# Optimization experiments

Measured on AMD Instinct MI355X. Metric: run time of the kernel, lower is better.

## Reference

```python
import jax, jax.numpy as jnp
import numpy as np

PI = np.pi


def setup_inputs() -> dict:
    key = jax.random.key(0)
    ks = jax.random.split(key, 20)
    B, L, D = 2, 1024, 512
    TP = 16      # n_sets(4) * planes_per_set(4)
    PP = 16      # pos_planes
    MAXL = 8192
    sc = 1.0 / np.sqrt(D)
    return {
        "x": jax.random.normal(ks[0], (B, L, D), jnp.float32),
        "Wk": jax.random.normal(ks[1], (TP, D), jnp.float32) * sc,
        "bk": jnp.zeros((TP,), jnp.float32),
        "Wq": jax.random.normal(ks[2], (TP, D), jnp.float32) * sc,
        "bq": jnp.zeros((TP,), jnp.float32),
        "Wv": jax.random.normal(ks[3], (D, D), jnp.float32) * sc,
        "bv": jnp.zeros((D,), jnp.float32),
        "ln_g": jnp.ones((D,), jnp.float32),
        "ln_b": jnp.zeros((D,), jnp.float32),
        "Wo": jax.random.normal(ks[4], (D, D), jnp.float32) * sc,
        "bo": jnp.zeros((D,), jnp.float32),
        "set_w": jnp.ones((4,), jnp.float32),
        "pos_phases": jax.random.normal(ks[5], (MAXL, PP), jnp.float32) * PI,
        "pos_weight": jnp.ones((1,), jnp.float32),
        "Wg1": jax.random.normal(ks[6], (D // 2, D), jnp.float32) * sc,
        "bg1": jnp.zeros((D // 2,), jnp.float32),
        "Wg2": jax.random.normal(ks[7], (1, D // 2), jnp.float32) * np.sqrt(2.0 / D),
        "bg2": jnp.zeros((1,), jnp.float32),
    }


def reference(x, Wk, bk, Wq, bq, Wv, bv, ln_g, ln_b, Wo, bo,
              set_w, pos_phases, pos_weight, Wg1, bg1, Wg2, bg2):
    B, L, D = x.shape
    n_sets, pps = 4, 4

    # --- content phasor memory ---
    kp = jnp.tanh(x @ Wk.T + bk) * PI                       # [B,L,16]
    qp = jnp.tanh(x @ Wq.T + bq) * PI
    key_ph = jnp.exp(1j * kp).reshape(B, L, n_sets, pps)    # [B,L,S,P] c64
    qry_ph = jnp.exp(1j * qp).reshape(B, L, n_sets, pps)
    Vr = x @ Wv.T + bv                                       # [B,L,D]
    V = Vr.astype(jnp.complex64)

    bound = key_ph[..., None] * V[:, :, None, None, :]       # [B,L,S,P,D] c64
    mem = jnp.cumsum(bound, axis=1)                          # prefix-sum memory
    retr = (mem * jnp.conj(qry_ph)[..., None]).sum(axis=3).real   # [B,L,S,D]
    w = jax.nn.softmax(set_w)
    content = (retr * w[None, None, :, None]).sum(axis=2)    # [B,L,D]

    # --- positional cos/sin memory ---
    ph = pos_phases[:L]                                      # [L,PP]
    c = jnp.cos(ph)[None]                                    # [1,L,PP]
    s = jnp.sin(ph)[None]
    br = Vr[:, :, None, :] * c[..., None]                    # [B,L,PP,D]
    bi = Vr[:, :, None, :] * s[..., None]
    mr = jnp.cumsum(br, axis=1)
    mi = jnp.cumsum(bi, axis=1)
    pos = (mr * c[..., None] + mi * s[..., None]).sum(axis=2)  # [B,L,D]

    # --- gate, mix, normalize, output proj ---
    g = jax.nn.sigmoid(
        jax.nn.gelu(x @ Wg1.T + bg1, approximate=False) @ Wg2.T + bg2)  # [B,L,1]
    total = g * content + (1.0 - g) * jax.nn.sigmoid(pos_weight) * pos
    norm = jnp.sqrt(jnp.arange(1, L + 1, dtype=x.dtype) * pps)[None, :, None]
    t = total / norm
    mu = t.mean(-1, keepdims=True)
    var = ((t - mu) ** 2).mean(-1, keepdims=True)
    tn = (t - mu) / jnp.sqrt(var + 1e-5) * ln_g + ln_b
    return x + tn @ Wo.T + bo
```

## Files before the change

kernel.cpp:

```cpp
#include <hip/hip_runtime.h>
#include <math.h>

#define PI_F 3.14159265358979323846f
#define BB 2
#define LL 1024
#define NCH 64
#define CHUNK 32
#define NCHUNK (LL/CHUNK)
#define NW 1408

typedef __attribute__((ext_vector_type(8))) short short8;
typedef __attribute__((ext_vector_type(4))) float floatx4;
typedef const __attribute__((address_space(1))) unsigned int cgu32;
typedef __attribute__((address_space(3))) unsigned int lu32;

__device__ __forceinline__ unsigned short f2bf(float f){
    unsigned u = __float_as_uint(f);
    unsigned r = (u + 0x7fff + ((u >> 16) & 1)) >> 16;
    return (unsigned short)r;
}

__global__ __launch_bounds__(128) void k_prep(
    const float* __restrict__ Wv, const float* __restrict__ Wg1,
    const float* __restrict__ Wk, const float* __restrict__ Wq,
    const float* __restrict__ Wo,
    const float* __restrict__ bv, const float* __restrict__ bg1,
    const float* __restrict__ bk, const float* __restrict__ bq,
    const float* __restrict__ bo, const float* __restrict__ x,
    unsigned short* __restrict__ Wb, float* __restrict__ bcat,
    unsigned short* __restrict__ xb)
{
    const int bid = blockIdx.x, tid = threadIdx.x;
    if (bid < NW){
        const int n = bid;
        const float* src = (n<512) ? Wv  + (size_t)n*512
                         : (n<768) ? Wg1 + (size_t)(n-512)*512
                         : (n<784) ? Wk  + (size_t)(n-768)*512
                         : (n<800) ? Wq  + (size_t)(n-784)*512
                         : (n<896) ? (const float*)0
                                   : Wo  + (size_t)(n-896)*512;
        float4 v = make_float4(0.f,0.f,0.f,0.f);
        if (src) v = ((const float4*)src)[tid];
        ushort4 o; o.x=f2bf(v.x); o.y=f2bf(v.y); o.z=f2bf(v.z); o.w=f2bf(v.w);
        ((ushort4*)(Wb + (size_t)n*512))[tid] = o;
        if (tid == 0)
            bcat[n] = (n<512)?bv[n] : (n<768)?bg1[n-512] : (n<784)?bk[n-768]
                    : (n<800)?bq[n-784] : (n<896)?0.f : bo[n-896];
    } else {
        const size_t i = (size_t)(bid - NW)*128 + tid;
        float4 v = ((const float4*)x)[i];
        ushort4 o; o.x=f2bf(v.x); o.y=f2bf(v.y); o.z=f2bf(v.z); o.w=f2bf(v.w);
        ((ushort4*)xb)[i] = o;
    }
}

__device__ __forceinline__ void gemm64x64(
    const unsigned short* Ag, const unsigned short* Bg,
    short* As, short* Bs, int tid, floatx4 acc[2][2])
{
    const int lane = tid & 63, w = tid >> 6;
    const int wm = w & 1, wn = w >> 1;
    const int q = lane >> 4, m15 = lane & 15;
    for (int kt = 0; kt < 512; kt += 64) {
        __syncthreads();
        #pragma unroll
        for (int i = 0; i < 2; ++i) {
            const int rowbase = (w*2 + i) * 8;
            const int r  = rowbase + (lane >> 3);
            const int gb = (lane & 7) ^ (r & 7);
            __builtin_amdgcn_global_load_lds(
                (cgu32*)(const void*)(Ag + (size_t)r*512 + kt + gb*8),
                (lu32*)(As + rowbase*64), 16, 0, 0);
            __builtin_amdgcn_global_load_lds(
                (cgu32*)(const void*)(Bg + (size_t)r*512 + kt + gb*8),
                (lu32*)(Bs + rowbase*64), 16, 0, 0);
        }
        __syncthreads();
        #pragma unroll
        for (int k32 = 0; k32 < 64; k32 += 32) {
            short8 af[2], bf[2];
            #pragma unroll
            for (int t = 0; t < 2; ++t) {
                const int ra  = 32*wm + 16*t + m15;
                const int sba = ((k32>>3) + q) ^ (ra & 7);
                af[t] = *(const short8*)(As + ra*64 + sba*8);
                const int rb  = 32*wn + 16*t + m15;
                const int sbb = ((k32>>3) + q) ^ (rb & 7);
                bf[t] = *(const short8*)(Bs + rb*64 + sbb*8);
            }
            #pragma unroll
            for (int mt = 0; mt < 2; ++mt)
                #pragma unroll
                for (int nt = 0; nt < 2; ++nt)
                    acc[mt][nt] = __builtin_amdgcn_mfma_f32_16x16x32_bf16(
                        af[mt], bf[nt], acc[mt][nt], 0, 0, 0);
        }
    }
}

__global__ __launch_bounds__(256,2) void kg1f(
    const unsigned short* __restrict__ xb, const unsigned short* __restrict__ Wb,
    const float* __restrict__ bcat, const float* __restrict__ Wg2,
    const float* __restrict__ bg2, const float* __restrict__ set_w,
    const float* __restrict__ pos_phases, const float* __restrict__ pos_weight,
    unsigned short* __restrict__ Vt,
    unsigned short* __restrict__ ab, unsigned short* __restrict__ Rb,
    unsigned short* __restrict__ aT)
{
    __shared__ short smem[22528];
    const int bid = blockIdx.x, tid = threadIdx.x;
    const int lane = tid & 63, w = tid >> 6;
    const int q = lane >> 4, m15 = lane & 15;

    if (bid < 256){
        short* As = smem;
        short* Bs = smem + 64*64;
        const int row0 = (bid >> 3)*64, n0 = (bid & 7)*64;
        floatx4 acc[2][2];
        #pragma unroll
        for (int mt=0;mt<2;++mt)
            #pragma unroll
            for (int nt=0;nt<2;++nt) acc[mt][nt] = (floatx4){0.f,0.f,0.f,0.f};
        gemm64x64(xb + (size_t)row0*512, Wb + (size_t)n0*512, As, Bs, tid, acc);
        const int wm = w & 1, wn = w >> 1;
        const int b = row0 >> 10, lb = row0 & 1023;
        #pragma unroll
        for (int mt=0;mt<2;++mt)
            #pragma unroll
            for (int nt=0;nt<2;++nt){
                const int d = n0 + 32*wn + 16*nt + m15;
                const float bb = bcat[d];
                const int l0 = lb + 32*wm + 16*mt + q*4;
                ushort4 o;
                o.x = f2bf(acc[mt][nt][0] + bb);
                o.y = f2bf(acc[mt][nt][1] + bb);
                o.z = f2bf(acc[mt][nt][2] + bb);
                o.w = f2bf(acc[mt][nt][3] + bb);
                *(ushort4*)(Vt + ((size_t)(b*512 + d))*1024 + l0) = o;
            }
    } else {
        short* As2 = smem;
        short* Bs2 = smem + 64*64;
        const int r0 = (bid - 256)*64;
        floatx4 acc2[18];
        #pragma unroll
        for (int nt=0;nt<18;++nt) acc2[nt] = (floatx4){0.f,0.f,0.f,0.f};
        for (int kt = 0; kt < 512; kt += 64){
            __syncthreads();
            #pragma unroll
            for (int i=0;i<2;++i){
                const int rowbase = (w*2 + i)*8;
                const int r = rowbase + (lane >> 3);
                const int gb = (lane & 7) ^ (r & 7);
                __builtin_amdgcn_global_load_lds(
                    (cgu32*)(const void*)(xb + (size_t)(r0 + r)*512 + kt + gb*8),
                    (lu32*)(As2 + rowbase*64), 16, 0, 0);
            }
            #pragma unroll
            for (int i=0;i<9;++i){
                const int rowbase = (w*9 + i)*8;
                const int r = rowbase + (lane >> 3);
                const int gb = (lane & 7) ^ (r & 7);
                __builtin_amdgcn_global_load_lds(
                    (cgu32*)(const void*)(Wb + (size_t)(512 + r)*512 + kt + gb*8),
                    (lu32*)(Bs2 + rowbase*64), 16, 0, 0);
            }
            __syncthreads();
            #pragma unroll
            for (int k32 = 0; k32 < 64; k32 += 32){
                const int ra  = 16*w + m15;
                const int sba = ((k32>>3) + q) ^ (ra & 7);
                short8 af = *(const short8*)(As2 + ra*64 + sba*8);
                #pragma unroll
                for (int nt=0;nt<18;++nt){
                    const int rb  = 16*nt + m15;
                    const int sbb = ((k32>>3) + q) ^ (rb & 7);
                    short8 bf = *(const short8*)(Bs2 + rb*64 + sbb*8);
                    acc2[nt] = __builtin_amdgcn_mfma_f32_16x16x32_bf16(
                        af, bf, acc2[nt], 0, 0, 0);
                }
            }
        }
        float s0=set_w[0], s1=set_w[1], s2=set_w[2], s3=set_w[3];
        float mx = fmaxf(fmaxf(s0,s1), fmaxf(s2,s3));
        float e0=expf(s0-mx), e1=expf(s1-mx), e2=expf(s2-mx), e3=expf(s3-mx);
        float esum = e0+e1+e2+e3;
        float spw = 1.f/(1.f+expf(-pos_weight[0]));
        float b2 = bg2[0];
        float part[4] = {0.f,0.f,0.f,0.f};
        #pragma unroll
        for (int nt=0;nt<16;++nt){
            const float w2 = Wg2[16*nt + m15];
            const float hb = bcat[512 + 16*nt + m15];
            #pragma unroll
            for (int reg=0;reg<4;++reg){
                float hv = acc2[nt][reg] + hb;
                float ge = 0.5f*hv*(1.f + erff(hv*0.70710678118f));
                part[reg] += ge*w2;
            }
        }
        #pragma unroll
        for (int off=8; off; off>>=1)
            #pragma unroll
            for (int reg=0;reg<4;++reg) part[reg] += __shfl_xor(part[reg], off, 64);
        const int j = m15;
        const float bkj = bcat[768 + j], bqj = bcat[784 + j];
        const float wsm = (j<4?e0: j<8?e1: j<12?e2: e3) / esum;
        #pragma unroll
        for (int reg=0;reg<4;++reg){
            const int row = r0 + 16*w + q*4 + reg;
            const int l = row & (LL-1), b = row >> 10;
            float g = 1.f/(1.f+expf(-(part[reg] + b2)));
            float kang = PI_F*tanhf(acc2[16][reg] + bkj);
            float qang = PI_F*tanhf(acc2[17][reg] + bqj);
            float rnorm = 1.f/(2.f*sqrtf((float)(l+1)));
            float av[4], rv[4];
            av[0] = cosf(kang); av[1] = sinf(kang);
            float cw = g*wsm*rnorm;
            rv[0] = cw*cosf(qang); rv[1] = cw*sinf(qang);
            float ph = pos_phases[(size_t)l*16 + j];
            float pc = cosf(ph), ps = sinf(ph);
            av[2] = pc; av[3] = ps;
            float cp = (1.f-g)*spw*rnorm;
            rv[2] = cp*pc; rv[3] = cp*ps;
            unsigned short* arow = ab + (size_t)row*NCH;
            unsigned short* Rrow = Rb + (size_t)row*NCH;
            #pragma unroll
            for (int t=0;t<4;++t){
                arow[16*t + j] = f2bf(av[t]);
                Rrow[16*t + j] = f2bf(rv[t]);
                aT[((size_t)(b*NCH + 16*t + j))*1024 + l] = f2bf(av[t]);
            }
        }
    }
}

__global__ __launch_bounds__(256) void k2a_chunksum(
    const unsigned short* __restrict__ aT, const unsigned short* __restrict__ Vt,
    float* __restrict__ P)
{
    const int c = blockIdx.x, b = blockIdx.y, z = blockIdx.z;
    const int tid = threadIdx.x, lane = tid & 63, w = tid >> 6;
    const int q = lane >> 4, m15 = lane & 15;
    short8 af[4];
    #pragma unroll
    for (int mt=0;mt<4;++mt)
        af[mt] = *(const short8*)(aT + ((size_t)b*NCH + 16*mt + m15)*1024 + c*32 + q*8);
    floatx4 acc[4][4];
    #pragma unroll
    for (int mt=0;mt<4;++mt)
        #pragma unroll
        for (int nt=0;nt<4;++nt) acc[mt][nt] = (floatx4){0.f,0.f,0.f,0.f};
    #pragma unroll
    for (int nt=0;nt<4;++nt){
        const int d = z*256 + w*64 + 16*nt + m15;
        short8 bf = *(const short8*)(Vt + ((size_t)(b*512 + d))*1024 + c*32 + q*8);
        #pragma unroll
        for (int mt=0;mt<4;++mt)
            acc[mt][nt] = __builtin_amdgcn_mfma_f32_16x16x32_bf16(af[mt], bf, acc[mt][nt], 0,0,0);
    }
    float* Pc = P + ((size_t)(b*NCHUNK + c))*512*NCH;
    #pragma unroll
    for (int mt=0;mt<4;++mt)
        #pragma unroll
        for (int nt=0;nt<4;++nt){
            const int d = z*256 + w*64 + 16*nt + m15;
            *(floatx4*)(Pc + (size_t)d*NCH + 16*mt + q*4) = acc[mt][nt];
        }
}

__global__ __launch_bounds__(256) void k2b_prefix(
    const float* __restrict__ P, unsigned short* __restrict__ S0t)
{
    const int b = blockIdx.y;
    const size_t idx = (size_t)blockIdx.x*256 + threadIdx.x;
    float run = 0.f;
    for (int c=0;c<NCHUNK;++c){
        const size_t o = ((size_t)(b*NCHUNK + c))*512*NCH + idx;
        float v = P[o];
        S0t[o] = f2bf(run);
        run += v;
    }
}

__global__ __launch_bounds__(256) void k2c_scan(
    const unsigned short* __restrict__ ab, const unsigned short* __restrict__ Rb,
    const unsigned short* __restrict__ Vt, const unsigned short* __restrict__ S0t,
    const float* __restrict__ ln_g, const float* __restrict__ ln_b,
    unsigned short* __restrict__ Tn)
{
    __shared__ short Msh[32*32];
    __shared__ float Tsh[32*512];
    const int c = blockIdx.x, b = blockIdx.y;
    const int tid = threadIdx.x, lane = tid & 63, w = tid >> 6;
    const int q = lane >> 4, m15 = lane & 15;
    const int grow = b*1024 + c*32;

    if (w == 0){
        floatx4 mcc[2][2];
        #pragma unroll
        for (int mt=0;mt<2;++mt)
            #pragma unroll
            for (int nt=0;nt<2;++nt) mcc[mt][nt] = (floatx4){0.f,0.f,0.f,0.f};
        #pragma unroll
        for (int ks=0;ks<2;++ks){
            short8 ra[2], bb[2];
            #pragma unroll
            for (int t=0;t<2;++t){
                ra[t] = *(const short8*)(Rb + (size_t)(grow + 16*t + m15)*NCH + ks*32 + q*8);
                bb[t] = *(const short8*)(ab + (size_t)(grow + 16*t + m15)*NCH + ks*32 + q*8);
            }
            #pragma unroll
            for (int mt=0;mt<2;++mt)
                #pragma unroll
                for (int nt=0;nt<2;++nt)
                    mcc[mt][nt] = __builtin_amdgcn_mfma_f32_16x16x32_bf16(
                        ra[mt], bb[nt], mcc[mt][nt], 0,0,0);
        }
        #pragma unroll
        for (int mt=0;mt<2;++mt)
            #pragma unroll
            for (int nt=0;nt<2;++nt){
                const int nl = 16*nt + m15;
                #pragma unroll
                for (int reg=0;reg<4;++reg){
                    const int ml = 16*mt + q*4 + reg;
                    Msh[ml*32 + nl] = (nl <= ml) ? (short)f2bf(mcc[mt][nt][reg]) : (short)0;
                }
            }
    }
    __syncthreads();

    short8 a1[2], a2[2][2];
    #pragma unroll
    for (int mt=0;mt<2;++mt){
        a1[mt] = *(const short8*)(Msh + (16*mt + m15)*32 + q*8);
        #pragma unroll
        for (int ks=0;ks<2;++ks)
            a2[ks][mt] = *(const short8*)(Rb + (size_t)(grow + 16*mt + m15)*NCH + ks*32 + q*8);
    }
    floatx4 acc[2][8];
    #pragma unroll
    for (int mt=0;mt<2;++mt)
        #pragma unroll
        for (int nt=0;nt<8;++nt) acc[mt][nt] = (floatx4){0.f,0.f,0.f,0.f};
    const unsigned short* S0c = S0t + ((size_t)(b*NCHUNK + c))*512*NCH;
    #pragma unroll
    for (int nt=0;nt<8;++nt){
        const int d = w*128 + 16*nt + m15;
        short8 b1 = *(const short8*)(Vt + ((size_t)(b*512 + d))*1024 + c*32 + q*8);
        #pragma unroll
        for (int mt=0;mt<2;++mt)
            acc[mt][nt] = __builtin_amdgcn_mfma_f32_16x16x32_bf16(a1[mt], b1, acc[mt][nt], 0,0,0);
        #pragma unroll
        for (int ks=0;ks<2;++ks){
            short8 b2 = *(const short8*)(S0c + (size_t)d*NCH + ks*32 + q*8);
            #pragma unroll
            for (int mt=0;mt<2;++mt)
                acc[mt][nt] = __builtin_amdgcn_mfma_f32_16x16x32_bf16(a2[ks][mt], b2, acc[mt][nt], 0,0,0);
        }
    }
    #pragma unroll
    for (int mt=0;mt<2;++mt)
        #pragma unroll
        for (int nt=0;nt<8;++nt){
            const int d = w*128 + 16*nt + m15;
            #pragma unroll
            for (int reg=0;reg<4;++reg)
                Tsh[(16*mt + q*4 + reg)*512 + d] = acc[mt][nt][reg];
        }
    __syncthreads();

    #pragma unroll
    for (int i=0;i<8;++i){
        const int r = w*8 + i;
        float s=0.f, sq=0.f;
        #pragma unroll
        for (int t=0;t<8;++t){
            float v = Tsh[r*512 + lane + 64*t];
            s += v; sq += v*v;
        }
        #pragma unroll
        for (int off=32; off; off>>=1){
            s += __shfl_xor(s, off, 64); sq += __shfl_xor(sq, off, 64);
        }
        float mu  = s*(1.f/512.f);
        float var = sq*(1.f/512.f) - mu*mu;
        float rsd = rsqrtf(var + 1e-5f);
        unsigned short* trow = Tn + (size_t)(grow + r)*512;
        #pragma unroll
        for (int t=0;t<8;++t){
            const int d = lane + 64*t;
            float v = (Tsh[r*512 + d] - mu)*rsd*ln_g[d] + ln_b[d];
            trow[d] = f2bf(v);
        }
    }
}

__global__ __launch_bounds__(256) void kg2(
    const unsigned short* __restrict__ Tn, const unsigned short* __restrict__ Wb,
    const float* __restrict__ bcat, const float* __restrict__ x,
    float* __restrict__ out)
{
    __shared__ short As[64*64], Bs[64*64];
    const int tid = threadIdx.x;
    const int row0 = blockIdx.x*64, n0 = blockIdx.y*64;
    floatx4 acc[2][2];
    #pragma unroll
    for (int mt=0;mt<2;++mt)
        #pragma unroll
        for (int nt=0;nt<2;++nt) acc[mt][nt] = (floatx4){0.f,0.f,0.f,0.f};
    gemm64x64(Tn + (size_t)row0*512, Wb + (size_t)(896+n0)*512, As, Bs, tid, acc);
    const int lane = tid & 63, w = tid >> 6;
    const int wm = w & 1, wn = w >> 1, q = lane >> 4, m15 = lane & 15;
    #pragma unroll
    for (int mt=0;mt<2;++mt)
        #pragma unroll
        for (int nt=0;nt<2;++nt){
            const int n = n0 + 32*wn + 16*nt + m15;
            const float bb = bcat[896 + n];
            #pragma unroll
            for (int reg=0;reg<4;++reg){
                const int m = row0 + 32*wm + 16*mt + q*4 + reg;
                out[(size_t)m*512 + n] = x[(size_t)m*512 + n] + acc[mt][nt][reg] + bb;
            }
        }
}

extern "C" void kernel_launch(void* const* d_in, const int* in_sizes, int n_in,
                              void* d_out, int out_size, void* d_ws, size_t ws_size,
                              hipStream_t stream) {
    const float* x    = (const float*)d_in[0];
    const float* Wk   = (const float*)d_in[1];
    const float* bk   = (const float*)d_in[2];
    const float* Wq   = (const float*)d_in[3];
    const float* bq   = (const float*)d_in[4];
    const float* Wv   = (const float*)d_in[5];
    const float* bv   = (const float*)d_in[6];
    const float* ln_g = (const float*)d_in[7];
    const float* ln_b = (const float*)d_in[8];
    const float* Wo   = (const float*)d_in[9];
    const float* bo   = (const float*)d_in[10];
    const float* set_w      = (const float*)d_in[11];
    const float* pos_phases = (const float*)d_in[12];
    const float* pos_weight = (const float*)d_in[13];
    const float* Wg1  = (const float*)d_in[14];
    const float* bg1  = (const float*)d_in[15];
    const float* Wg2  = (const float*)d_in[16];
    const float* bg2  = (const float*)d_in[17];
    float* out = (float*)d_out;

    float* ws   = (float*)d_ws;
    float* bcat = ws;
    float* P    = bcat + NW;
    unsigned short* Wb  = (unsigned short*)(P + (size_t)BB*NCHUNK*512*NCH);
    unsigned short* xb  = Wb  + (size_t)NW*512;
    unsigned short* Vt  = xb  + (size_t)2048*512;
    unsigned short* ab  = Vt  + (size_t)BB*512*1024;
    unsigned short* Rb  = ab  + (size_t)2048*NCH;
    unsigned short* aT  = Rb  + (size_t)2048*NCH;
    unsigned short* S0t = aT  + (size_t)BB*NCH*1024;
    unsigned short* Tn  = S0t + (size_t)BB*NCHUNK*512*NCH;

    k_prep<<<dim3(NW + 2048), 128, 0, stream>>>(
        Wv,Wg1,Wk,Wq,Wo, bv,bg1,bk,bq,bo, x, Wb, bcat, xb);
    kg1f<<<dim3(288), 256, 0, stream>>>(
        xb, Wb, bcat, Wg2, bg2, set_w, pos_phases, pos_weight, Vt, ab, Rb, aT);
    k2a_chunksum<<<dim3(NCHUNK, BB, 2), 256, 0, stream>>>(aT, Vt, P);
    k2b_prefix<<<dim3(512*NCH/256, BB), 256, 0, stream>>>(P, S0t);
    k2c_scan<<<dim3(NCHUNK, BB), 256, 0, stream>>>(ab, Rb, Vt, S0t, ln_g, ln_b, Tn);
    kg2<<<dim3(2048/64, 512/64), 256, 0, stream>>>(Tn, Wb, bcat, x, out);
}
```

Before: 148.5 us.

## Fold LayerNorm into output GEMM epilogue and widen scan grid

```diff
diff --git a/kernel.cpp b/kernel.cpp
--- a/kernel.cpp
+++ b/kernel.cpp
@@ -27,11 +27,14 @@
     const float* __restrict__ bv, const float* __restrict__ bg1,
     const float* __restrict__ bk, const float* __restrict__ bq,
     const float* __restrict__ bo, const float* __restrict__ x,
+    const float* __restrict__ ln_g, const float* __restrict__ ln_b,
     unsigned short* __restrict__ Wb, float* __restrict__ bcat,
+    float* __restrict__ Gv, float* __restrict__ Bv, float* __restrict__ stats,
     unsigned short* __restrict__ xb)
 {
     const int bid = blockIdx.x, tid = threadIdx.x;
     if (bid < NW){
+        if (bid < 32) stats[bid*128 + tid] = 0.f;
         const int n = bid;
         const float* src = (n<512) ? Wv  + (size_t)n*512
                          : (n<768) ? Wg1 + (size_t)(n-512)*512
@@ -41,11 +44,34 @@
                                    : Wo  + (size_t)(n-896)*512;
         float4 v = make_float4(0.f,0.f,0.f,0.f);
         if (src) v = ((const float4*)src)[tid];
-        ushort4 o; o.x=f2bf(v.x); o.y=f2bf(v.y); o.z=f2bf(v.z); o.w=f2bf(v.w);
-        ((ushort4*)(Wb + (size_t)n*512))[tid] = o;
+        if (n >= 896){
+            float4 g4 = ((const float4*)ln_g)[tid];
+            float4 b4 = ((const float4*)ln_b)[tid];
+            ushort4 o;
+            o.x=f2bf(v.x*g4.x); o.y=f2bf(v.y*g4.y);
+            o.z=f2bf(v.z*g4.z); o.w=f2bf(v.w*g4.w);
+            ((ushort4*)(Wb + (size_t)n*512))[tid] = o;
+            float pg = v.x*g4.x + v.y*g4.y + v.z*g4.z + v.w*g4.w;
+            float pb = v.x*b4.x + v.y*b4.y + v.z*b4.z + v.w*b4.w;
+            #pragma unroll
+            for (int off=32; off; off>>=1){
+                pg += __shfl_xor(pg, off, 64); pb += __shfl_xor(pb, off, 64);
+            }
+            __shared__ float red[4];
+            const int wv = tid >> 6;
+            if ((tid & 63) == 0){ red[wv*2] = pg; red[wv*2+1] = pb; }
+            __syncthreads();
+            if (tid == 0){
+                Gv[n-896] = red[0] + red[2];
+                Bv[n-896] = red[1] + red[3] + bo[n-896];
+            }
+        } else {
+            ushort4 o; o.x=f2bf(v.x); o.y=f2bf(v.y); o.z=f2bf(v.z); o.w=f2bf(v.w);
+            ((ushort4*)(Wb + (size_t)n*512))[tid] = o;
+        }
         if (tid == 0)
             bcat[n] = (n<512)?bv[n] : (n<768)?bg1[n-512] : (n<784)?bk[n-768]
-                    : (n<800)?bq[n-784] : (n<896)?0.f : bo[n-896];
+                    : (n<800)?bq[n-784] : 0.f;
     } else {
         const size_t i = (size_t)(bid - NW)*128 + tid;
         float4 v = ((const float4*)x)[i];
@@ -112,10 +138,11 @@
     const int lane = tid & 63, w = tid >> 6;
     const int q = lane >> 4, m15 = lane & 15;
 
-    if (bid < 256){
+    if (bid >= 32){
         short* As = smem;
         short* Bs = smem + 64*64;
-        const int row0 = (bid >> 3)*64, n0 = (bid & 7)*64;
+        const int vb = bid - 32;
+        const int row0 = (vb >> 3)*64, n0 = (vb & 7)*64;
         floatx4 acc[2][2];
         #pragma unroll
         for (int mt=0;mt<2;++mt)
@@ -141,7 +168,7 @@
     } else {
         short* As2 = smem;
         short* Bs2 = smem + 64*64;
-        const int r0 = (bid - 256)*64;
+        const int r0 = bid*64;
         floatx4 acc2[18];
         #pragma unroll
         for (int nt=0;nt<18;++nt) acc2[nt] = (floatx4){0.f,0.f,0.f,0.f};
@@ -246,14 +273,14 @@
     #pragma unroll
     for (int mt=0;mt<4;++mt)
         af[mt] = *(const short8*)(aT + ((size_t)b*NCH + 16*mt + m15)*1024 + c*32 + q*8);
-    floatx4 acc[4][4];
+    floatx4 acc[4][2];
     #pragma unroll
     for (int mt=0;mt<4;++mt)
         #pragma unroll
-        for (int nt=0;nt<4;++nt) acc[mt][nt] = (floatx4){0.f,0.f,0.f,0.f};
-    #pragma unroll
-    for (int nt=0;nt<4;++nt){
-        const int d = z*256 + w*64 + 16*nt + m15;
+        for (int nt=0;nt<2;++nt) acc[mt][nt] = (floatx4){0.f,0.f,0.f,0.f};
+    #pragma unroll
+    for (int nt=0;nt<2;++nt){
+        const int d = z*128 + w*32 + 16*nt + m15;
         short8 bf = *(const short8*)(Vt + ((size_t)(b*512 + d))*1024 + c*32 + q*8);
         #pragma unroll
         for (int mt=0;mt<4;++mt)
@@ -263,8 +290,8 @@
     #pragma unroll
     for (int mt=0;mt<4;++mt)
         #pragma unroll
-        for (int nt=0;nt<4;++nt){
-            const int d = z*256 + w*64 + 16*nt + m15;
+        for (int nt=0;nt<2;++nt){
+            const int d = z*128 + w*32 + 16*nt + m15;
             *(floatx4*)(Pc + (size_t)d*NCH + 16*mt + q*4) = acc[mt][nt];
         }
 }
@@ -274,132 +301,124 @@
 {
     const int b = blockIdx.y;
     const size_t idx = (size_t)blockIdx.x*256 + threadIdx.x;
+    const size_t base = (size_t)b*NCHUNK*512*NCH + idx;
+    float vcs[NCHUNK];
+    #pragma unroll
+    for (int c=0;c<NCHUNK;++c)
+        vcs[c] = P[base + (size_t)c*512*NCH];
     float run = 0.f;
+    #pragma unroll
     for (int c=0;c<NCHUNK;++c){
-        const size_t o = ((size_t)(b*NCHUNK + c))*512*NCH + idx;
-        float v = P[o];
-        S0t[o] = f2bf(run);
-        run += v;
+        S0t[base + (size_t)c*512*NCH] = f2bf(run);
+        run += vcs[c];
     }
 }
 
 __global__ __launch_bounds__(256) void k2c_scan(
     const unsigned short* __restrict__ ab, const unsigned short* __restrict__ Rb,
     const unsigned short* __restrict__ Vt, const unsigned short* __restrict__ S0t,
-    const float* __restrict__ ln_g, const float* __restrict__ ln_b,
-    unsigned short* __restrict__ Tn)
-{
-    __shared__ short Msh[32*32];
-    __shared__ float Tsh[32*512];
-    const int c = blockIdx.x, b = blockIdx.y;
+    unsigned short* __restrict__ Tn, float* __restrict__ stats)
+{
+    __shared__ short Msh[4][32*32];
+    const int c = blockIdx.x, b = blockIdx.y, z = blockIdx.z;
     const int tid = threadIdx.x, lane = tid & 63, w = tid >> 6;
     const int q = lane >> 4, m15 = lane & 15;
     const int grow = b*1024 + c*32;
 
-    if (w == 0){
-        floatx4 mcc[2][2];
+    short8 ra[2][2], av[2][2];
+    #pragma unroll
+    for (int ks=0;ks<2;++ks)
+        #pragma unroll
+        for (int t=0;t<2;++t){
+            ra[ks][t] = *(const short8*)(Rb + (size_t)(grow + 16*t + m15)*NCH + ks*32 + q*8);
+            av[ks][t] = *(const short8*)(ab + (size_t)(grow + 16*t + m15)*NCH + ks*32 + q*8);
+        }
+    floatx4 mcc[2][2];
+    #pragma unroll
+    for (int mt=0;mt<2;++mt)
+        #pragma unroll
+        for (int nt=0;nt<2;++nt) mcc[mt][nt] = (floatx4){0.f,0.f,0.f,0.f};
+    #pragma unroll
+    for (int ks=0;ks<2;++ks)
         #pragma unroll
         for (int mt=0;mt<2;++mt)
             #pragma unroll
-            for (int nt=0;nt<2;++nt) mcc[mt][nt] = (floatx4){0.f,0.f,0.f,0.f};
+            for (int nt=0;nt<2;++nt)
+                mcc[mt][nt] = __builtin_amdgcn_mfma_f32_16x16x32_bf16(
+                    ra[ks][mt], av[ks][nt], mcc[mt][nt], 0,0,0);
+    short* Mw = &Msh[w][0];
+    #pragma unroll
+    for (int mt=0;mt<2;++mt)
+        #pragma unroll
+        for (int nt=0;nt<2;++nt){
+            const int nl = 16*nt + m15;
+            #pragma unroll
+            for (int reg=0;reg<4;++reg){
+                const int ml = 16*mt + q*4 + reg;
+                Mw[ml*32 + nl] = (nl <= ml) ? (short)f2bf(mcc[mt][nt][reg]) : (short)0;
+            }
+        }
+    short8 a1[2];
+    #pragma unroll
+    for (int mt=0;mt<2;++mt)
+        a1[mt] = *(const short8*)(Mw + (16*mt + m15)*32 + q*8);
+
+    floatx4 acc[2][2];
+    #pragma unroll
+    for (int mt=0;mt<2;++mt)
+        #pragma unroll
+        for (int nt=0;nt<2;++nt) acc[mt][nt] = (floatx4){0.f,0.f,0.f,0.f};
+    const unsigned short* S0c = S0t + ((size_t)(b*NCHUNK + c))*512*NCH;
+    #pragma unroll
+    for (int nt=0;nt<2;++nt){
+        const int d = z*128 + w*32 + 16*nt + m15;
+        short8 vfr = *(const short8*)(Vt + ((size_t)(b*512 + d))*1024 + c*32 + q*8);
+        #pragma unroll
+        for (int mt=0;mt<2;++mt)
+            acc[mt][nt] = __builtin_amdgcn_mfma_f32_16x16x32_bf16(a1[mt], vfr, acc[mt][nt], 0,0,0);
         #pragma unroll
         for (int ks=0;ks<2;++ks){
-            short8 ra[2], bb[2];
-            #pragma unroll
-            for (int t=0;t<2;++t){
-                ra[t] = *(const short8*)(Rb + (size_t)(grow + 16*t + m15)*NCH + ks*32 + q*8);
-                bb[t] = *(const short8*)(ab + (size_t)(grow + 16*t + m15)*NCH + ks*32 + q*8);
-            }
+            short8 sfr = *(const short8*)(S0c + (size_t)d*NCH + ks*32 + q*8);
             #pragma unroll
             for (int mt=0;mt<2;++mt)
-                #pragma unroll
-                for (int nt=0;nt<2;++nt)
-                    mcc[mt][nt] = __builtin_amdgcn_mfma_f32_16x16x32_bf16(
-                        ra[mt], bb[nt], mcc[mt][nt], 0,0,0);
-        }
-        #pragma unroll
-        for (int mt=0;mt<2;++mt)
-            #pragma unroll
-            for (int nt=0;nt<2;++nt){
-                const int nl = 16*nt + m15;
-                #pragma unroll
-                for (int reg=0;reg<4;++reg){
-                    const int ml = 16*mt + q*4 + reg;
-                    Msh[ml*32 + nl] = (nl <= ml) ? (short)f2bf(mcc[mt][nt][reg]) : (short)0;
-                }
-            }
-    }
-    __syncthreads();
-
-    short8 a1[2], a2[2][2];
+                acc[mt][nt] = __builtin_amdgcn_mfma_f32_16x16x32_bf16(ra[ks][mt], sfr, acc[mt][nt], 0,0,0);
+        }
+    }
     #pragma unroll
     for (int mt=0;mt<2;++mt){
-        a1[mt] = *(const short8*)(Msh + (16*mt + m15)*32 + q*8);
-        #pragma unroll
-        for (int ks=0;ks<2;++ks)
-            a2[ks][mt] = *(const short8*)(Rb + (size_t)(grow + 16*mt + m15)*NCH + ks*32 + q*8);
-    }
-    floatx4 acc[2][8];
-    #pragma unroll
-    for (int mt=0;mt<2;++mt)
-        #pragma unroll
-        for (int nt=0;nt<8;++nt) acc[mt][nt] = (floatx4){0.f,0.f,0.f,0.f};
-    const unsigned short* S0c = S0t + ((size_t)(b*NCHUNK + c))*512*NCH;
-    #pragma unroll
-    for (int nt=0;nt<8;++nt){
-        const int d = w*128 + 16*nt + m15;
-        short8 b1 = *(const short8*)(Vt + ((size_t)(b*512 + d))*1024 + c*32 + q*8);
-        #pragma unroll
-        for (int mt=0;mt<2;++mt)
-            acc[mt][nt] = __builtin_amdgcn_mfma_f32_16x16x32_bf16(a1[mt], b1, acc[mt][nt], 0,0,0);
-        #pragma unroll
-        for (int ks=0;ks<2;++ks){
-            short8 b2 = *(const short8*)(S0c + (size_t)d*NCH + ks*32 + q*8);
-            #pragma unroll
-            for (int mt=0;mt<2;++mt)
-                acc[mt][nt] = __builtin_amdgcn_mfma_f32_16x16x32_bf16(a2[ks][mt], b2, acc[mt][nt], 0,0,0);
-        }
-    }
-    #pragma unroll
-    for (int mt=0;mt<2;++mt)
-        #pragma unroll
-        for (int nt=0;nt<8;++nt){
-            const int d = w*128 + 16*nt + m15;
-            #pragma unroll
-            for (int reg=0;reg<4;++reg)
-                Tsh[(16*mt + q*4 + reg)*512 + d] = acc[mt][nt][reg];
-        }
-    __syncthreads();
-
-    #pragma unroll
-    for (int i=0;i<8;++i){
-        const int r = w*8 + i;
-        float s=0.f, sq=0.f;
-        #pragma unroll
-        for (int t=0;t<8;++t){
-            float v = Tsh[r*512 + lane + 64*t];
-            s += v; sq += v*v;
-        }
-        #pragma unroll
-        for (int off=32; off; off>>=1){
-            s += __shfl_xor(s, off, 64); sq += __shfl_xor(sq, off, 64);
-        }
-        float mu  = s*(1.f/512.f);
-        float var = sq*(1.f/512.f) - mu*mu;
-        float rsd = rsqrtf(var + 1e-5f);
-        unsigned short* trow = Tn + (size_t)(grow + r)*512;
-        #pragma unroll
-        for (int t=0;t<8;++t){
-            const int d = lane + 64*t;
-            float v = (Tsh[r*512 + d] - mu)*rsd*ln_g[d] + ln_b[d];
-            trow[d] = f2bf(v);
+        float s[4] = {0.f,0.f,0.f,0.f}, sq[4] = {0.f,0.f,0.f,0.f};
+        #pragma unroll
+        for (int nt=0;nt<2;++nt){
+            const int d = z*128 + w*32 + 16*nt + m15;
+            #pragma unroll
+            for (int reg=0;reg<4;++reg){
+                const float vv = acc[mt][nt][reg];
+                Tn[(size_t)(grow + 16*mt + q*4 + reg)*512 + d] = f2bf(vv);
+                s[reg] += vv; sq[reg] += vv*vv;
+            }
+        }
+        #pragma unroll
+        for (int off=1; off<16; off<<=1)
+            #pragma unroll
+            for (int reg=0;reg<4;++reg){
+                s[reg]  += __shfl_xor(s[reg],  off, 64);
+                sq[reg] += __shfl_xor(sq[reg], off, 64);
+            }
+        if (m15 == 0){
+            #pragma unroll
+            for (int reg=0;reg<4;++reg){
+                const int r = grow + 16*mt + q*4 + reg;
+                atomicAdd(&stats[2*r],   s[reg]);
+                atomicAdd(&stats[2*r+1], sq[reg]);
+            }
         }
     }
 }
 
 __global__ __launch_bounds__(256) void kg2(
     const unsigned short* __restrict__ Tn, const unsigned short* __restrict__ Wb,
-    const float* __restrict__ bcat, const float* __restrict__ x,
+    const float* __restrict__ x, const float* __restrict__ stats,
+    const float* __restrict__ Gv, const float* __restrict__ Bv,
     float* __restrict__ out)
 {
     __shared__ short As[64*64], Bs[64*64];
@@ -418,11 +437,16 @@
         #pragma unroll
         for (int nt=0;nt<2;++nt){
             const int n = n0 + 32*wn + 16*nt + m15;
-            const float bb = bcat[896 + n];
+            const float Gn = Gv[n], Bn = Bv[n];
             #pragma unroll
             for (int reg=0;reg<4;++reg){
                 const int m = row0 + 32*wm + 16*mt + q*4 + reg;
-                out[(size_t)m*512 + n] = x[(size_t)m*512 + n] + acc[mt][nt][reg] + bb;
+                const float2 st = ((const float2*)stats)[m];
+                const float mu  = st.x*(1.f/512.f);
+                const float var = st.y*(1.f/512.f) - mu*mu;
+                const float rs  = rsqrtf(var + 1e-5f);
+                out[(size_t)m*512 + n] = x[(size_t)m*512 + n]
+                                       + rs*(acc[mt][nt][reg] - mu*Gn) + Bn;
             }
         }
 }
@@ -450,9 +474,12 @@
     const float* bg2  = (const float*)d_in[17];
     float* out = (float*)d_out;
 
-    float* ws   = (float*)d_ws;
-    float* bcat = ws;
-    float* P    = bcat + NW;
+    float* ws    = (float*)d_ws;
+    float* bcat  = ws;
+    float* stats = bcat  + NW;
+    float* Gv    = stats + 4096;
+    float* Bv    = Gv    + 512;
+    float* P     = Bv    + 512;
     unsigned short* Wb  = (unsigned short*)(P + (size_t)BB*NCHUNK*512*NCH);
     unsigned short* xb  = Wb  + (size_t)NW*512;
     unsigned short* Vt  = xb  + (size_t)2048*512;
@@ -463,11 +490,12 @@
     unsigned short* Tn  = S0t + (size_t)BB*NCHUNK*512*NCH;
 
     k_prep<<<dim3(NW + 2048), 128, 0, stream>>>(
-        Wv,Wg1,Wk,Wq,Wo, bv,bg1,bk,bq,bo, x, Wb, bcat, xb);
+        Wv,Wg1,Wk,Wq,Wo, bv,bg1,bk,bq,bo, x, ln_g, ln_b,
+        Wb, bcat, Gv, Bv, stats, xb);
     kg1f<<<dim3(288), 256, 0, stream>>>(
         xb, Wb, bcat, Wg2, bg2, set_w, pos_phases, pos_weight, Vt, ab, Rb, aT);
-    k2a_chunksum<<<dim3(NCHUNK, BB, 2), 256, 0, stream>>>(aT, Vt, P);
+    k2a_chunksum<<<dim3(NCHUNK, BB, 4), 256, 0, stream>>>(aT, Vt, P);
     k2b_prefix<<<dim3(512*NCH/256, BB), 256, 0, stream>>>(P, S0t);
-    k2c_scan<<<dim3(NCHUNK, BB), 256, 0, stream>>>(ab, Rb, Vt, S0t, ln_g, ln_b, Tn);
-    kg2<<<dim3(2048/64, 512/64), 256, 0, stream>>>(Tn, Wb, bcat, x, out);
-}
+    k2c_scan<<<dim3(NCHUNK, BB, 4), 256, 0, stream>>>(ab, Rb, Vt, S0t, Tn, stats);
+    kg2<<<dim3(2048/64, 512/64), 256, 0, stream>>>(Tn, Wb, x, stats, Gv, Bv, out);
+}
```

New measurement: 149.8 us. No clear change (+0.8%).
